# Kernel optimization log

Hardware: AMD Instinct MI355X
Metric: run time of the kernel (lower is better)

## Reference

```python
import jax, jax.numpy as jnp
import numpy as np

D = 512      # d_model
H = 8        # n_heads
DH = D // H  # d_head
WIN = 128    # window radius
FF = 4 * D   # ffn hidden
B, T = 4, 2048
EPS = 1e-5


def _ln(x, g, b):
    mu = jnp.mean(x, axis=-1, keepdims=True)
    var = jnp.mean((x - mu) ** 2, axis=-1, keepdims=True)
    return (x - mu) * jax.lax.rsqrt(var + EPS) * g + b


def _rope(x):
    # standard rotate-half RoPE over the full d_model dim (applied to ln(x)
    # before q/k/v projections, as in the source module)
    t, d = x.shape[-2], x.shape[-1]
    half = d // 2
    inv_freq = 1.0 / (10000.0 ** (jnp.arange(half, dtype=jnp.float32) / half))
    ang = jnp.arange(t, dtype=jnp.float32)[:, None] * inv_freq[None, :]  # (T, half)
    cos, sin = jnp.cos(ang), jnp.sin(ang)
    x1, x2 = x[..., :half], x[..., half:]
    return jnp.concatenate([x1 * cos - x2 * sin, x1 * sin + x2 * cos], axis=-1)


def setup_inputs() -> dict:
    key = jax.random.key(0)
    ks = jax.random.split(key, 16)
    s = 0.02
    inp = {
        "x": jax.random.normal(ks[0], (B, T, D), dtype=jnp.float32),
        "Wq": jax.random.normal(ks[1], (D, D), dtype=jnp.float32) * s,
        "bq": jnp.zeros((D,), jnp.float32),
        "Wk": jax.random.normal(ks[2], (D, D), dtype=jnp.float32) * s,
        "bk": jnp.zeros((D,), jnp.float32),
        "Wv": jax.random.normal(ks[3], (D, D), dtype=jnp.float32) * s,
        "bv": jnp.zeros((D,), jnp.float32),
        "Wo": jax.random.normal(ks[4], (D, D), dtype=jnp.float32) * s,
        "bo": jnp.zeros((D,), jnp.float32),
        "ln_g": jnp.ones((D,), jnp.float32),
        "ln_b": jnp.zeros((D,), jnp.float32),
        "ffln_g": jnp.ones((D,), jnp.float32),
        "ffln_b": jnp.zeros((D,), jnp.float32),
        "W1": jax.random.normal(ks[5], (D, FF), dtype=jnp.float32) * s,
        "b1": jnp.zeros((FF,), jnp.float32),
        "W2": jax.random.normal(ks[6], (FF, D), dtype=jnp.float32) * s,
        "b2": jnp.zeros((D,), jnp.float32),
    }
    return inp


def reference(x, Wq, bq, Wk, bk, Wv, bv, Wo, bo, ln_g, ln_b, ffln_g, ffln_b, W1, b1, W2, b2):
    b, t, d = x.shape
    h = _rope(_ln(x, ln_g, ln_b))
    q = (h @ Wq + bq).reshape(b, t, H, DH).transpose(0, 2, 1, 3)  # (B,H,T,DH)
    k = (h @ Wk + bk).reshape(b, t, H, DH).transpose(0, 2, 1, 3)
    v = (h @ Wv + bv).reshape(b, t, H, DH).transpose(0, 2, 1, 3)

    scores = jnp.einsum("bhqd,bhkd->bhqk", q, k) / jnp.sqrt(jnp.float32(DH))
    # Faithful to source local_mask semantics under torch SDPA bool-mask
    # convention (True = attend): attention is ALLOWED where |i-j| > window.
    idx = jnp.arange(t)
    allowed = jnp.abs(idx[:, None] - idx[None, :]) > WIN  # (T,T) bool
    scores = jnp.where(allowed, scores, -jnp.inf)
    attn = jax.nn.softmax(scores, axis=-1)
    o = jnp.einsum("bhqk,bhkd->bhqd", attn, v)
    o = o.transpose(0, 2, 1, 3).reshape(b, t, d)
    x = x + (o @ Wo + bo)

    # source applies self.ln AND the ff's internal LayerNorm back-to-back
    f = _ln(_ln(x, ln_g, ln_b), ffln_g, ffln_b)
    f = jax.nn.gelu(f @ W1 + b1, approximate=False) @ W2 + b2
    return x + f
```

## Files before the change

kernel.cpp:

```cpp
#include <hip/hip_runtime.h>
#include <cmath>

typedef __bf16 bf16x8 __attribute__((ext_vector_type(8)));
typedef float  f32x4  __attribute__((ext_vector_type(4)));
typedef float  f32x16 __attribute__((ext_vector_type(16)));
typedef int    i32x4  __attribute__((ext_vector_type(4)));

#define MFMA(a, b, c)   __builtin_amdgcn_mfma_f32_16x16x32_bf16((a), (b), (c), 0, 0, 0)
#define MFMA32(a, b, c) __builtin_amdgcn_mfma_f32_32x32x16_bf16((a), (b), (c), 0, 0, 0)

static __device__ __forceinline__ unsigned fbits(float f) {
  union { float f; unsigned u; } v; v.f = f; return v.u;
}
static __device__ __forceinline__ __bf16 f2bf(float f) {
  unsigned u = fbits(f);
  unsigned r = u + 0x7fffu + ((u >> 16) & 1u);
  union { unsigned short u; __bf16 b; } o; o.u = (unsigned short)(r >> 16);
  return o.b;
}
static __device__ __forceinline__ unsigned pack2rn(float a, float b) {
  unsigned ua = fbits(a); ua = ua + 0x7fffu + ((ua >> 16) & 1u);
  unsigned ub = fbits(b); ub = ub + 0x7fffu + ((ub >> 16) & 1u);
  return __builtin_amdgcn_perm(ub, ua, 0x07060302);
}

typedef const __attribute__((address_space(1))) void* gas_t;
typedef __attribute__((address_space(3))) void* las_t;
static __device__ __forceinline__ void load_lds16(const __bf16* g, __bf16* l) {
  __builtin_amdgcn_global_load_lds((gas_t)g, (las_t)l, 16, 0, 0);
}

__global__ __launch_bounds__(256) void k_pre(
    const float* __restrict__ Wq, const float* __restrict__ Wk,
    const float* __restrict__ Wv, const float* __restrict__ Wo,
    const float* __restrict__ W1, const float* __restrict__ W2,
    __bf16* __restrict__ wqkv, __bf16* __restrict__ wo,
    __bf16* __restrict__ w1t, __bf16* __restrict__ w2t,
    const float* __restrict__ x, const float* __restrict__ g,
    const float* __restrict__ b, __bf16* __restrict__ h) {
  if (blockIdx.x < 12288) {
    int idx = blockIdx.x * 256 + threadIdx.x;
    const float* src; __bf16* dst; int off, logK, N;
    if (idx < 1048576) {
      int which = idx >> 18; off = idx & 262143; logK = 9; N = 512;
      src = which == 0 ? Wq : which == 1 ? Wk : which == 2 ? Wv : Wo;
      dst = which < 3 ? wqkv + which * 262144 : wo;
    } else if (idx < 2097152) {
      off = idx - 1048576; logK = 9; N = 2048; src = W1; dst = w1t;
    } else {
      off = idx - 2097152; logK = 11; N = 512; src = W2; dst = w2t;
    }
    int n = off >> logK, k = off & ((1 << logK) - 1);
    dst[off] = f2bf(src[(size_t)k * N + n]);
    return;
  }
  int n = blockIdx.x - 12288, tid = threadIdx.x;
  const float* row = x + (size_t)n * 512;
  float v1 = row[tid], v2 = row[tid + 256];
  float s = v1 + v2, ss = v1 * v1 + v2 * v2;
  #pragma unroll
  for (int off = 1; off < 64; off <<= 1) { s += __shfl_xor(s, off, 64); ss += __shfl_xor(ss, off, 64); }
  __shared__ float red[2][4];
  if ((tid & 63) == 0) { red[0][tid >> 6] = s; red[1][tid >> 6] = ss; }
  __syncthreads();
  s  = red[0][0] + red[0][1] + red[0][2] + red[0][3];
  ss = red[1][0] + red[1][1] + red[1][2] + red[1][3];
  float mu = s * (1.f / 512.f);
  float var = ss * (1.f / 512.f) - mu * mu;
  float rs = rsqrtf(var + 1e-5f);
  float y1 = (v1 - mu) * rs * g[tid] + b[tid];
  float y2 = (v2 - mu) * rs * g[tid + 256] + b[tid + 256];
  int t = n & 2047;
  float inv = __expf(-(float)tid * 0.03597789207803197f);
  float ang = (float)t * inv;
  float sn, c;
  __sincosf(ang, &sn, &c);
  h[(size_t)n * 512 + tid]       = f2bf(y1 * c - y2 * sn);
  h[(size_t)n * 512 + tid + 256] = f2bf(y1 * sn + y2 * c);
}

template <int K>
static __device__ __forceinline__ void gemm128(const __bf16* __restrict__ A,
                                               const __bf16* __restrict__ Bt,
                                               f32x4 (&acc)[2][4]) {
  __shared__ __bf16 lA[128 * 64];
  __shared__ __bf16 lB[128 * 64];
  int bm = blockIdx.x & 63, bn = blockIdx.x >> 6;
  int tid = threadIdx.x, w = tid >> 6, lane = tid & 63;
  int l16 = lane & 15, quad = lane >> 4;
  int wr = (w & 3) * 32, wc = (w >> 2) * 64;
  int srow = w * 8 + (lane >> 3);
  int sg = (lane & 7) ^ (srow & 7);
  const __bf16* ga = A  + (size_t)(bm * 128 + srow) * K + sg * 8;
  const __bf16* gb = Bt + (size_t)(bn * 128 + srow) * K + sg * 8;
  __bf16* saw = lA + w * 512;
  __bf16* sbw = lB + w * 512;
  #pragma unroll
  for (int i = 0; i < 2; ++i)
    #pragma unroll
    for (int j = 0; j < 4; ++j) acc[i][j] = {0.f, 0.f, 0.f, 0.f};
  const size_t rstep = (size_t)64 * K;
  for (int k0 = 0; k0 < K; k0 += 64) {
    load_lds16(ga + k0,         saw);
    load_lds16(ga + k0 + rstep, saw + 4096);
    load_lds16(gb + k0,         sbw);
    load_lds16(gb + k0 + rstep, sbw + 4096);
    __syncthreads();
    #pragma unroll
    for (int kk = 0; kk < 2; ++kk) {
      int gg = kk * 4 + quad;
      bf16x8 af[2], bfr[4];
      #pragma unroll
      for (int i = 0; i < 2; ++i) {
        int row = wr + i * 16 + l16;
        __builtin_memcpy(&af[i], &lA[row * 64 + ((gg ^ (row & 7)) * 8)], 16);
      }
      #pragma unroll
      for (int j = 0; j < 4; ++j) {
        int row = wc + j * 16 + l16;
        __builtin_memcpy(&bfr[j], &lB[row * 64 + ((gg ^ (row & 7)) * 8)], 16);
      }
      #pragma unroll
      for (int i = 0; i < 2; ++i)
        #pragma unroll
        for (int j = 0; j < 4; ++j) acc[i][j] = MFMA(af[i], bfr[j], acc[i][j]);
    }
    __syncthreads();
  }
}

#define G128_EPILOG_IDX                                 \
  int bm = blockIdx.x & 63, bn = blockIdx.x >> 6;       \
  int lane = threadIdx.x & 63, w = threadIdx.x >> 6;    \
  int l16 = lane & 15, quad = lane >> 4;                \
  int wr = (w & 3) * 32, wc = (w >> 2) * 64;

__global__ __launch_bounds__(512) void k_gemm_qkv(const __bf16* __restrict__ A,
                                                  const __bf16* __restrict__ Bt,
                                                  const float* __restrict__ bq,
                                                  const float* __restrict__ bk,
                                                  const float* __restrict__ bv,
                                                  __bf16* __restrict__ qo,
                                                  __bf16* __restrict__ ko,
                                                  __bf16* __restrict__ vT) {
  f32x4 acc[2][4];
  gemm128<512>(A, Bt, acc);
  G128_EPILOG_IDX
  int proj = bn >> 2;
  const float* bias = proj == 0 ? bq : (proj == 1 ? bk : bv);
  float scale = proj == 0 ? 0.125f : 1.f;
  if (proj < 2) {
    __bf16* dst = proj == 0 ? qo : ko;
    #pragma unroll
    for (int i = 0; i < 2; ++i)
      #pragma unroll
      for (int j = 0; j < 4; ++j)
        #pragma unroll
        for (int r = 0; r < 4; ++r) {
          int c = (bn * 128 + wc + j * 16 + l16) & 511;
          int m = bm * 128 + wr + i * 16 + quad * 4 + r;
          int bI = m >> 11, t = m & 2047;
          int head = c >> 6, dh = c & 63;
          dst[(((size_t)bI * 8 + head) * 2048 + t) * 64 + dh] = f2bf((acc[i][j][r] + bias[c]) * scale);
        }
  } else {
    #pragma unroll
    for (int i = 0; i < 2; ++i)
      #pragma unroll
      for (int j = 0; j < 4; ++j)
        #pragma unroll
        for (int r = 0; r < 4; ++r) {
          int c = (bn * 128 + wc + j * 16 + l16) & 511;
          int m = bm * 128 + wr + i * 16 + quad * 4 + r;
          int bI = m >> 11, t = m & 2047;
          int head = c >> 6, dh = c & 63;
          vT[(((size_t)bI * 8 + head) * 64 + dh) * 2048 + t] = f2bf(acc[i][j][r] + bias[c]);
        }
  }
}

template <int K, typename EPI>
static __device__ __forceinline__ void gemm64sk(const __bf16* __restrict__ A,
                                                const __bf16* __restrict__ Bt,
                                                EPI epi) {
  __shared__ __align__(16) char smem[64 * 128 * 2 * 2];
  __bf16* lA = (__bf16*)smem;
  __bf16* lB = lA + 64 * 128;
  int bm = blockIdx.x & 127, bn = blockIdx.x >> 7;
  int tid = threadIdx.x, w = tid >> 6, lane = tid & 63;
  int l16 = lane & 15, quad = lane >> 4;
  int pos = w & 3, half = w >> 2;
  int wr = (pos >> 1) * 32, wc = (pos & 1) * 32;
  int srow = tid >> 4;
  int sg = (tid & 15) ^ (srow & 15);
  const __bf16* ga = A  + (size_t)(bm * 64 + srow) * K + sg * 8;
  const __bf16* gb = Bt + (size_t)(bn * 64 + srow) * K + sg * 8;
  __bf16* sa = lA + w * 512;
  __bf16* sb = lB + w * 512;
  f32x4 acc[2][2];
  #pragma unroll
  for (int i = 0; i < 2; ++i)
    #pragma unroll
    for (int j = 0; j < 2; ++j) acc[i][j] = {0.f, 0.f, 0.f, 0.f};
  const size_t rstep = (size_t)32 * K;
  for (int k0 = 0; k0 < K; k0 += 128) {
    load_lds16(ga + k0,         sa);
    load_lds16(ga + k0 + rstep, sa + 4096);
    load_lds16(gb + k0,         sb);
    load_lds16(gb + k0 + rstep, sb + 4096);
    __syncthreads();
    #pragma unroll
    for (int kk = 0; kk < 2; ++kk) {
      int gg = half * 8 + kk * 4 + quad;
      bf16x8 af[2], bfr[2];
      #pragma unroll
      for (int i = 0; i < 2; ++i) {
        int row = wr + i * 16 + l16;
        __builtin_memcpy(&af[i], &lA[row * 128 + ((gg ^ (row & 15)) * 8)], 16);
      }
      #pragma unroll
      for (int j = 0; j < 2; ++j) {
        int row = wc + j * 16 + l16;
        __builtin_memcpy(&bfr[j], &lB[row * 128 + ((gg ^ (row & 15)) * 8)], 16);
      }
      #pragma unroll
      for (int i = 0; i < 2; ++i)
        #pragma unroll
        for (int j = 0; j < 2; ++j) acc[i][j] = MFMA(af[i], bfr[j], acc[i][j]);
    }
    __syncthreads();
  }
  float (*cbuf)[64][17] = (float(*)[64][17])smem;
  if (half) {
    #pragma unroll
    for (int i = 0; i < 2; ++i)
      #pragma unroll
      for (int j = 0; j < 2; ++j)
        #pragma unroll
        for (int r = 0; r < 4; ++r) cbuf[pos][lane][(i * 2 + j) * 4 + r] = acc[i][j][r];
  }
  __syncthreads();
  if (!half) {
    #pragma unroll
    for (int i = 0; i < 2; ++i)
      #pragma unroll
      for (int j = 0; j < 2; ++j)
        #pragma unroll
        for (int r = 0; r < 4; ++r) {
          float v = acc[i][j][r] + cbuf[pos][lane][(i * 2 + j) * 4 + r];
          int m = bm * 64 + wr + i * 16 + quad * 4 + r;
          int n = bn * 64 + wc + j * 16 + l16;
          epi(m, n, v);
        }
  }
}

__global__ __launch_bounds__(512) void k_gemm_oproj(const __bf16* __restrict__ A,
                                                    const __bf16* __restrict__ Bt,
                                                    const float* __restrict__ bo,
                                                    const float* __restrict__ xin,
                                                    float* __restrict__ x2) {
  gemm64sk<512>(A, Bt, [&](int m, int n, float v) {
    size_t idx = (size_t)m * 512 + n;
    x2[idx] = xin[idx] + v + bo[n];
  });
}

__global__ __launch_bounds__(512) void k_gemm_ffn2(const __bf16* __restrict__ A,
                                                   const __bf16* __restrict__ Bt,
                                                   const float* __restrict__ b2,
                                                   const float* __restrict__ x2,
                                                   float* __restrict__ out) {
  gemm64sk<2048>(A, Bt, [&](int m, int n, float v) {
    size_t idx = (size_t)m * 512 + n;
    out[idx] = x2[idx] + v + b2[n];
  });
}

__global__ __launch_bounds__(512) void k_attn(const __bf16* __restrict__ q,
                                              const __bf16* __restrict__ k,
                                              const __bf16* __restrict__ vT,
                                              __bf16* __restrict__ o) {
  __shared__ __align__(16) __bf16 Kt[64 * 64];
  __shared__ __align__(16) __bf16 Vt[64 * 64];
  __shared__ float cbuf[4][64][17];
  int bh = blockIdx.x >> 4, qblk = blockIdx.x & 15;
  int tid = threadIdx.x, w = tid >> 6, lane = tid & 63;
  int l32 = lane & 31, h32 = lane >> 5;
  int qw = w & 3, half = w >> 2, hoff = half * 32;
  int qB = qblk * 128;
  int q0 = qB + qw * 32;
  int qglob = q0 + l32;
  const __bf16* qb = q + (size_t)bh * 2048 * 64;
  const __bf16* kb = k + (size_t)bh * 2048 * 64;
  const __bf16* vb = vT + (size_t)bh * 64 * 2048;
  bf16x8 aq[4];
  #pragma unroll
  for (int i = 0; i < 4; ++i)
    aq[i] = *(const bf16x8*)(qb + (size_t)qglob * 64 + i * 16 + h32 * 8);
  f32x16 on0 = {0,0,0,0,0,0,0,0,0,0,0,0,0,0,0,0};
  f32x16 on1 = {0,0,0,0,0,0,0,0,0,0,0,0,0,0,0,0};
  float lsum = 0.f;
  int srow = w * 8 + (lane >> 3);
  int sg = (lane & 7) ^ (srow & 7);
  const __bf16* gk = kb + (size_t)srow * 64 + sg * 8;
  const __bf16* gv = vb + (size_t)srow * 2048 + sg * 8;
  __bf16* skw = Kt + w * 512;
  __bf16* svw = Vt + w * 512;

  for (int it = 0; it < 32; ++it) {
    int kt64 = it * 64;
    if ((unsigned)(kt64 - qB) <= 64u) continue;
    load_lds16(gk + (size_t)kt64 * 64, skw);
    load_lds16(gv + kt64, svw);
    __syncthreads();
    int myk0 = kt64 + hoff;
    bool skip = (q0 + 31 - myk0 <= 128) && (myk0 + 31 - q0 <= 128);
    if (!skip) {
      bool need_mask = !((myk0 >= q0 + 160) || (myk0 <= q0 - 160));
      f32x16 sc = {0,0,0,0,0,0,0,0,0,0,0,0,0,0,0,0};
      int krow = hoff + l32;
      #pragma unroll
      for (int i = 0; i < 4; ++i) {
        int gg = i * 2 + h32;
        bf16x8 bk;
        __builtin_memcpy(&bk, &Kt[krow * 64 + ((gg ^ (krow & 7)) * 8)], 16);
        sc = MFMA32(bk, aq[i], sc);
      }
      unsigned pk[8];
      #pragma unroll
      for (int g2 = 0; g2 < 8; ++g2) {
        int r0 = 2 * g2;
        float p0 = __expf(sc[r0]);
        float p1 = __expf(sc[r0 + 1]);
        if (need_mask) {
          int k0l = (r0 & 3) + 8 * (r0 >> 2) + 4 * h32;
          if ((unsigned)(qglob - (myk0 + k0l) + 128) <= 256u) p0 = 0.f;
          if ((unsigned)(qglob - (myk0 + k0l + 1) + 128) <= 256u) p1 = 0.f;
        }
        lsum += p0 + p1;
        pk[g2] = __builtin_amdgcn_perm(fbits(p1), fbits(p0), 0x07060302);
      }
      unsigned ex[8];
      #pragma unroll
      for (int g2 = 0; g2 < 8; ++g2) ex[g2] = (unsigned)__shfl_xor((int)pk[g2], 32);
      #pragma unroll
      for (int kk = 0; kk < 2; ++kk) {
        int o4 = kk * 4;
        i32x4 fi;
        fi.x = (int)(h32 ? ex[o4 + 2] : pk[o4 + 0]);
        fi.y = (int)(h32 ? ex[o4 + 3] : pk[o4 + 1]);
        fi.z = (int)(h32 ? pk[o4 + 2] : ex[o4 + 0]);
        fi.w = (int)(h32 ? pk[o4 + 3] : ex[o4 + 1]);
        bf16x8 pf;
        __builtin_memcpy(&pf, &fi, 16);
        int gg = half * 4 + kk * 2 + h32;
        bf16x8 bv0, bv1;
        __builtin_memcpy(&bv0, &Vt[l32 * 64 + ((gg ^ (l32 & 7)) * 8)], 16);
        __builtin_memcpy(&bv1, &Vt[(32 + l32) * 64 + ((gg ^ (l32 & 7)) * 8)], 16);
        on0 = MFMA32(bv0, pf, on0);
        on1 = MFMA32(bv1, pf, on1);
      }
    }
    __syncthreads();
  }
  if (half) {
    for (int i = 0; i < 16; ++i) cbuf[qw][lane][i] = on0[i];
  }
  __syncthreads();
  if (!half) {
    for (int i = 0; i < 16; ++i) on0[i] += cbuf[qw][lane][i];
  }
  __syncthreads();
  if (half) {
    for (int i = 0; i < 16; ++i) cbuf[qw][lane][i] = on1[i];
  }
  __syncthreads();
  if (!half) {
    for (int i = 0; i < 16; ++i) on1[i] += cbuf[qw][lane][i];
  }
  __syncthreads();
  if (half) {
    cbuf[qw][lane][0] = lsum;
  }
  __syncthreads();
  if (!half) {
    float s = lsum + cbuf[qw][lane][0];
    s += __shfl_xor(s, 32);
    float rl = 1.f / s;
    int bI = bh >> 3, head = bh & 7;
    __bf16* obase = o + ((size_t)(bI * 2048 + qglob)) * 512 + head * 64 + 4 * h32;
    #pragma unroll
    for (int g2 = 0; g2 < 4; ++g2) {
      int r0 = 4 * g2;
      int2 v0, v1;
      v0.x = (int)pack2rn(on0[r0] * rl, on0[r0 + 1] * rl);
      v0.y = (int)pack2rn(on0[r0 + 2] * rl, on0[r0 + 3] * rl);
      v1.x = (int)pack2rn(on1[r0] * rl, on1[r0 + 1] * rl);
      v1.y = (int)pack2rn(on1[r0 + 2] * rl, on1[r0 + 3] * rl);
      *(int2*)(obase + 8 * g2) = v0;
      *(int2*)(obase + 32 + 8 * g2) = v1;
    }
  }
}

__global__ __launch_bounds__(256) void k_ln_ln(const float* __restrict__ x2,
                                               const float* __restrict__ g1v,
                                               const float* __restrict__ b1v,
                                               const float* __restrict__ g2v,
                                               const float* __restrict__ b2v,
                                               __bf16* __restrict__ fout) {
  int n = blockIdx.x, tid = threadIdx.x;
  const float* row = x2 + (size_t)n * 512;
  float v1 = row[tid], v2 = row[tid + 256];
  __shared__ float red[2][4];
  float s = v1 + v2, ss = v1 * v1 + v2 * v2;
  #pragma unroll
  for (int off = 1; off < 64; off <<= 1) { s += __shfl_xor(s, off, 64); ss += __shfl_xor(ss, off, 64); }
  if ((tid & 63) == 0) { red[0][tid >> 6] = s; red[1][tid >> 6] = ss; }
  __syncthreads();
  s  = red[0][0] + red[0][1] + red[0][2] + red[0][3];
  ss = red[1][0] + red[1][1] + red[1][2] + red[1][3];
  float mu = s * (1.f / 512.f), var = ss * (1.f / 512.f) - mu * mu;
  float rs = rsqrtf(var + 1e-5f);
  float y1 = (v1 - mu) * rs * g1v[tid] + b1v[tid];
  float y2 = (v2 - mu) * rs * g1v[tid + 256] + b1v[tid + 256];
  __syncthreads();
  s = y1 + y2; ss = y1 * y1 + y2 * y2;
  #pragma unroll
  for (int off = 1; off < 64; off <<= 1) { s += __shfl_xor(s, off, 64); ss += __shfl_xor(ss, off, 64); }
  if ((tid & 63) == 0) { red[0][tid >> 6] = s; red[1][tid >> 6] = ss; }
  __syncthreads();
  s  = red[0][0] + red[0][1] + red[0][2] + red[0][3];
  ss = red[1][0] + red[1][1] + red[1][2] + red[1][3];
  float mu2 = s * (1.f / 512.f), var2 = ss * (1.f / 512.f) - mu2 * mu2;
  float rs2 = rsqrtf(var2 + 1e-5f);
  fout[(size_t)n * 512 + tid]       = f2bf((y1 - mu2) * rs2 * g2v[tid] + b2v[tid]);
  fout[(size_t)n * 512 + tid + 256] = f2bf((y2 - mu2) * rs2 * g2v[tid + 256] + b2v[tid + 256]);
}

__global__ __launch_bounds__(512) void k_gemm_ffn1(const __bf16* __restrict__ A,
                                                   const __bf16* __restrict__ Bt,
                                                   const float* __restrict__ b1,
                                                   __bf16* __restrict__ g1) {
  f32x4 acc[2][4];
  gemm128<512>(A, Bt, acc);
  G128_EPILOG_IDX
  #pragma unroll
  for (int i = 0; i < 2; ++i)
    #pragma unroll
    for (int j = 0; j < 4; ++j)
      #pragma unroll
      for (int r = 0; r < 4; ++r) {
        int n = bn * 128 + wc + j * 16 + l16;
        int m = bm * 128 + wr + i * 16 + quad * 4 + r;
        float t = acc[i][j][r] + b1[n];
        float ge = 0.5f * t * (1.f + erff(t * 0.7071067811865475f));
        g1[(size_t)m * 2048 + n] = f2bf(ge);
      }
}

extern "C" void kernel_launch(void* const* d_in, const int* in_sizes, int n_in,
                              void* d_out, int out_size, void* d_ws, size_t ws_size,
                              hipStream_t stream) {
  (void)in_sizes; (void)n_in; (void)out_size; (void)ws_size;
  const float* x   = (const float*)d_in[0];
  const float* Wq  = (const float*)d_in[1];
  const float* bq  = (const float*)d_in[2];
  const float* Wk  = (const float*)d_in[3];
  const float* bk  = (const float*)d_in[4];
  const float* Wv  = (const float*)d_in[5];
  const float* bv  = (const float*)d_in[6];
  const float* Wo  = (const float*)d_in[7];
  const float* bo  = (const float*)d_in[8];
  const float* lng = (const float*)d_in[9];
  const float* lnb = (const float*)d_in[10];
  const float* ffg = (const float*)d_in[11];
  const float* ffb = (const float*)d_in[12];
  const float* W1  = (const float*)d_in[13];
  const float* b1  = (const float*)d_in[14];
  const float* W2  = (const float*)d_in[15];
  const float* b2  = (const float*)d_in[16];
  float* out = (float*)d_out;

  char* ws = (char*)d_ws;
  __bf16* h    = (__bf16*)(ws);
  __bf16* qb   = (__bf16*)(ws + (size_t)8 * 1024 * 1024);
  __bf16* kb   = (__bf16*)(ws + (size_t)16 * 1024 * 1024);
  __bf16* vT   = (__bf16*)(ws + (size_t)24 * 1024 * 1024);
  float*  x2   = (float*)(ws + (size_t)32 * 1024 * 1024);
  __bf16* fb   = (__bf16*)(ws + (size_t)48 * 1024 * 1024);
  __bf16* wqkv = (__bf16*)(ws + (size_t)56 * 1024 * 1024);
  __bf16* wo   = wqkv + 3 * 512 * 512;
  __bf16* w1t  = wo + 512 * 512;
  __bf16* w2t  = w1t + 512 * 2048;
  __bf16* g1   = (__bf16*)(ws);

  k_pre<<<12288 + 8192, 256, 0, stream>>>(Wq, Wk, Wv, Wo, W1, W2, wqkv, wo, w1t, w2t,
                                          x, lng, lnb, h);
  k_gemm_qkv<<<64 * 12, 512, 0, stream>>>(h, wqkv, bq, bk, bv, qb, kb, vT);
  k_attn<<<32 * 16, 512, 0, stream>>>(qb, kb, vT, h);
  k_gemm_oproj<<<128 * 8, 512, 0, stream>>>(h, wo, bo, x, x2);
  k_ln_ln<<<8192, 256, 0, stream>>>(x2, lng, lnb, ffg, ffb, fb);
  k_gemm_ffn1<<<64 * 16, 512, 0, stream>>>(fb, w1t, b1, g1);
  k_gemm_ffn2<<<128 * 8, 512, 0, stream>>>(g1, w2t, b2, x2, out);
}
```

Before: 277.0 us.

## Switch QKV and FFN1 GEMMs to 64-tile split-K kernel, bf16 residual, exp2 softmax

Drops the 128x128 GEMM path and runs the QKV and FFN1 projections through the 64x64 split-K GEMM with more blocks. The Q scale is folded into a log2(e)/8 factor so attention can use a native exp2 in place of __expf. The intermediate residual x2 is stored as bf16 rather than fp32, cutting traffic for the LN and FFN2 epilogues but adding rounding error to the residual stream. The smaller tiles raise block count and occupancy at the cost of less operand reuse per block.

```diff
diff --git a/kernel.cpp b/kernel.cpp
--- a/kernel.cpp
+++ b/kernel.cpp
@@ -22,6 +22,13 @@
   unsigned ua = fbits(a); ua = ua + 0x7fffu + ((ua >> 16) & 1u);
   unsigned ub = fbits(b); ub = ub + 0x7fffu + ((ub >> 16) & 1u);
   return __builtin_amdgcn_perm(ub, ua, 0x07060302);
+}
+static __device__ __forceinline__ float fexp2(float x) {
+#if __has_builtin(__builtin_amdgcn_exp2f)
+  return __builtin_amdgcn_exp2f(x);
+#else
+  return exp2f(x);
+#endif
 }
 
 typedef const __attribute__((address_space(1))) void* gas_t;
@@ -77,106 +84,6 @@
   __sincosf(ang, &sn, &c);
   h[(size_t)n * 512 + tid]       = f2bf(y1 * c - y2 * sn);
   h[(size_t)n * 512 + tid + 256] = f2bf(y1 * sn + y2 * c);
-}
-
-template <int K>
-static __device__ __forceinline__ void gemm128(const __bf16* __restrict__ A,
-                                               const __bf16* __restrict__ Bt,
-                                               f32x4 (&acc)[2][4]) {
-  __shared__ __bf16 lA[128 * 64];
-  __shared__ __bf16 lB[128 * 64];
-  int bm = blockIdx.x & 63, bn = blockIdx.x >> 6;
-  int tid = threadIdx.x, w = tid >> 6, lane = tid & 63;
-  int l16 = lane & 15, quad = lane >> 4;
-  int wr = (w & 3) * 32, wc = (w >> 2) * 64;
-  int srow = w * 8 + (lane >> 3);
-  int sg = (lane & 7) ^ (srow & 7);
-  const __bf16* ga = A  + (size_t)(bm * 128 + srow) * K + sg * 8;
-  const __bf16* gb = Bt + (size_t)(bn * 128 + srow) * K + sg * 8;
-  __bf16* saw = lA + w * 512;
-  __bf16* sbw = lB + w * 512;
-  #pragma unroll
-  for (int i = 0; i < 2; ++i)
-    #pragma unroll
-    for (int j = 0; j < 4; ++j) acc[i][j] = {0.f, 0.f, 0.f, 0.f};
-  const size_t rstep = (size_t)64 * K;
-  for (int k0 = 0; k0 < K; k0 += 64) {
-    load_lds16(ga + k0,         saw);
-    load_lds16(ga + k0 + rstep, saw + 4096);
-    load_lds16(gb + k0,         sbw);
-    load_lds16(gb + k0 + rstep, sbw + 4096);
-    __syncthreads();
-    #pragma unroll
-    for (int kk = 0; kk < 2; ++kk) {
-      int gg = kk * 4 + quad;
-      bf16x8 af[2], bfr[4];
-      #pragma unroll
-      for (int i = 0; i < 2; ++i) {
-        int row = wr + i * 16 + l16;
-        __builtin_memcpy(&af[i], &lA[row * 64 + ((gg ^ (row & 7)) * 8)], 16);
-      }
-      #pragma unroll
-      for (int j = 0; j < 4; ++j) {
-        int row = wc + j * 16 + l16;
-        __builtin_memcpy(&bfr[j], &lB[row * 64 + ((gg ^ (row & 7)) * 8)], 16);
-      }
-      #pragma unroll
-      for (int i = 0; i < 2; ++i)
-        #pragma unroll
-        for (int j = 0; j < 4; ++j) acc[i][j] = MFMA(af[i], bfr[j], acc[i][j]);
-    }
-    __syncthreads();
-  }
-}
-
-#define G128_EPILOG_IDX                                 \
-  int bm = blockIdx.x & 63, bn = blockIdx.x >> 6;       \
-  int lane = threadIdx.x & 63, w = threadIdx.x >> 6;    \
-  int l16 = lane & 15, quad = lane >> 4;                \
-  int wr = (w & 3) * 32, wc = (w >> 2) * 64;
-
-__global__ __launch_bounds__(512) void k_gemm_qkv(const __bf16* __restrict__ A,
-                                                  const __bf16* __restrict__ Bt,
-                                                  const float* __restrict__ bq,
-                                                  const float* __restrict__ bk,
-                                                  const float* __restrict__ bv,
-                                                  __bf16* __restrict__ qo,
-                                                  __bf16* __restrict__ ko,
-                                                  __bf16* __restrict__ vT) {
-  f32x4 acc[2][4];
-  gemm128<512>(A, Bt, acc);
-  G128_EPILOG_IDX
-  int proj = bn >> 2;
-  const float* bias = proj == 0 ? bq : (proj == 1 ? bk : bv);
-  float scale = proj == 0 ? 0.125f : 1.f;
-  if (proj < 2) {
-    __bf16* dst = proj == 0 ? qo : ko;
-    #pragma unroll
-    for (int i = 0; i < 2; ++i)
-      #pragma unroll
-      for (int j = 0; j < 4; ++j)
-        #pragma unroll
-        for (int r = 0; r < 4; ++r) {
-          int c = (bn * 128 + wc + j * 16 + l16) & 511;
-          int m = bm * 128 + wr + i * 16 + quad * 4 + r;
-          int bI = m >> 11, t = m & 2047;
-          int head = c >> 6, dh = c & 63;
-          dst[(((size_t)bI * 8 + head) * 2048 + t) * 64 + dh] = f2bf((acc[i][j][r] + bias[c]) * scale);
-        }
-  } else {
-    #pragma unroll
-    for (int i = 0; i < 2; ++i)
-      #pragma unroll
-      for (int j = 0; j < 4; ++j)
-        #pragma unroll
-        for (int r = 0; r < 4; ++r) {
-          int c = (bn * 128 + wc + j * 16 + l16) & 511;
-          int m = bm * 128 + wr + i * 16 + quad * 4 + r;
-          int bI = m >> 11, t = m & 2047;
-          int head = c >> 6, dh = c & 63;
-          vT[(((size_t)bI * 8 + head) * 64 + dh) * 2048 + t] = f2bf(acc[i][j][r] + bias[c]);
-        }
-  }
 }
 
 template <int K, typename EPI>
@@ -255,25 +162,58 @@
   }
 }
 
+__global__ __launch_bounds__(512) void k_gemm_qkv(const __bf16* __restrict__ A,
+                                                  const __bf16* __restrict__ Bt,
+                                                  const float* __restrict__ bq,
+                                                  const float* __restrict__ bk,
+                                                  const float* __restrict__ bv,
+                                                  __bf16* __restrict__ qo,
+                                                  __bf16* __restrict__ ko,
+                                                  __bf16* __restrict__ vT) {
+  gemm64sk<512>(A, Bt, [&](int m, int n, float v) {
+    int proj = n >> 9, c = n & 511;
+    int bI = m >> 11, t = m & 2047;
+    int head = c >> 6, dh = c & 63;
+    if (proj == 0) {
+      qo[(((size_t)bI * 8 + head) * 2048 + t) * 64 + dh] = f2bf((v + bq[c]) * 0.18033688011112042f);
+    } else if (proj == 1) {
+      ko[(((size_t)bI * 8 + head) * 2048 + t) * 64 + dh] = f2bf(v + bk[c]);
+    } else {
+      vT[(((size_t)bI * 8 + head) * 64 + dh) * 2048 + t] = f2bf(v + bv[c]);
+    }
+  });
+}
+
 __global__ __launch_bounds__(512) void k_gemm_oproj(const __bf16* __restrict__ A,
                                                     const __bf16* __restrict__ Bt,
                                                     const float* __restrict__ bo,
                                                     const float* __restrict__ xin,
-                                                    float* __restrict__ x2) {
+                                                    __bf16* __restrict__ x2) {
   gemm64sk<512>(A, Bt, [&](int m, int n, float v) {
     size_t idx = (size_t)m * 512 + n;
-    x2[idx] = xin[idx] + v + bo[n];
+    x2[idx] = f2bf(xin[idx] + v + bo[n]);
+  });
+}
+
+__global__ __launch_bounds__(512) void k_gemm_ffn1(const __bf16* __restrict__ A,
+                                                   const __bf16* __restrict__ Bt,
+                                                   const float* __restrict__ b1,
+                                                   __bf16* __restrict__ g1) {
+  gemm64sk<512>(A, Bt, [&](int m, int n, float v) {
+    float t = v + b1[n];
+    float ge = 0.5f * t * (1.f + erff(t * 0.7071067811865475f));
+    g1[(size_t)m * 2048 + n] = f2bf(ge);
   });
 }
 
 __global__ __launch_bounds__(512) void k_gemm_ffn2(const __bf16* __restrict__ A,
                                                    const __bf16* __restrict__ Bt,
                                                    const float* __restrict__ b2,
-                                                   const float* __restrict__ x2,
+                                                   const __bf16* __restrict__ x2,
                                                    float* __restrict__ out) {
   gemm64sk<2048>(A, Bt, [&](int m, int n, float v) {
     size_t idx = (size_t)m * 512 + n;
-    out[idx] = x2[idx] + v + b2[n];
+    out[idx] = (float)x2[idx] + v + b2[n];
   });
 }
 
@@ -331,8 +271,8 @@
       #pragma unroll
       for (int g2 = 0; g2 < 8; ++g2) {
         int r0 = 2 * g2;
-        float p0 = __expf(sc[r0]);
-        float p1 = __expf(sc[r0 + 1]);
+        float p0 = fexp2(sc[r0]);
+        float p1 = fexp2(sc[r0 + 1]);
         if (need_mask) {
           int k0l = (r0 & 3) + 8 * (r0 >> 2) + 4 * h32;
           if ((unsigned)(qglob - (myk0 + k0l) + 128) <= 256u) p0 = 0.f;
@@ -404,14 +344,14 @@
   }
 }
 
-__global__ __launch_bounds__(256) void k_ln_ln(const float* __restrict__ x2,
+__global__ __launch_bounds__(256) void k_ln_ln(const __bf16* __restrict__ x2,
                                                const float* __restrict__ g1v,
                                                const float* __restrict__ b1v,
                                                const float* __restrict__ g2v,
                                                const float* __restrict__ b2v,
                                                __bf16* __restrict__ fout) {
   int n = blockIdx.x, tid = threadIdx.x;
-  const float* row = x2 + (size_t)n * 512;
+  const __bf16* row = x2 + (size_t)n * 512;
   float v1 = row[tid], v2 = row[tid + 256];
   __shared__ float red[2][4];
   float s = v1 + v2, ss = v1 * v1 + v2 * v2;
@@ -437,27 +377,6 @@
   float rs2 = rsqrtf(var2 + 1e-5f);
   fout[(size_t)n * 512 + tid]       = f2bf((y1 - mu2) * rs2 * g2v[tid] + b2v[tid]);
   fout[(size_t)n * 512 + tid + 256] = f2bf((y2 - mu2) * rs2 * g2v[tid + 256] + b2v[tid + 256]);
-}
-
-__global__ __launch_bounds__(512) void k_gemm_ffn1(const __bf16* __restrict__ A,
-                                                   const __bf16* __restrict__ Bt,
-                                                   const float* __restrict__ b1,
-                                                   __bf16* __restrict__ g1) {
-  f32x4 acc[2][4];
-  gemm128<512>(A, Bt, acc);
-  G128_EPILOG_IDX
-  #pragma unroll
-  for (int i = 0; i < 2; ++i)
-    #pragma unroll
-    for (int j = 0; j < 4; ++j)
-      #pragma unroll
-      for (int r = 0; r < 4; ++r) {
-        int n = bn * 128 + wc + j * 16 + l16;
-        int m = bm * 128 + wr + i * 16 + quad * 4 + r;
-        float t = acc[i][j][r] + b1[n];
-        float ge = 0.5f * t * (1.f + erff(t * 0.7071067811865475f));
-        g1[(size_t)m * 2048 + n] = f2bf(ge);
-      }
 }
 
 extern "C" void kernel_launch(void* const* d_in, const int* in_sizes, int n_in,
@@ -488,7 +407,7 @@
   __bf16* qb   = (__bf16*)(ws + (size_t)8 * 1024 * 1024);
   __bf16* kb   = (__bf16*)(ws + (size_t)16 * 1024 * 1024);
   __bf16* vT   = (__bf16*)(ws + (size_t)24 * 1024 * 1024);
-  float*  x2   = (float*)(ws + (size_t)32 * 1024 * 1024);
+  __bf16* x2   = (__bf16*)(ws + (size_t)32 * 1024 * 1024);
   __bf16* fb   = (__bf16*)(ws + (size_t)48 * 1024 * 1024);
   __bf16* wqkv = (__bf16*)(ws + (size_t)56 * 1024 * 1024);
   __bf16* wo   = wqkv + 3 * 512 * 512;
@@ -498,10 +417,10 @@
 
   k_pre<<<12288 + 8192, 256, 0, stream>>>(Wq, Wk, Wv, Wo, W1, W2, wqkv, wo, w1t, w2t,
                                           x, lng, lnb, h);
-  k_gemm_qkv<<<64 * 12, 512, 0, stream>>>(h, wqkv, bq, bk, bv, qb, kb, vT);
+  k_gemm_qkv<<<24 * 128, 512, 0, stream>>>(h, wqkv, bq, bk, bv, qb, kb, vT);
   k_attn<<<32 * 16, 512, 0, stream>>>(qb, kb, vT, h);
-  k_gemm_oproj<<<128 * 8, 512, 0, stream>>>(h, wo, bo, x, x2);
+  k_gemm_oproj<<<8 * 128, 512, 0, stream>>>(h, wo, bo, x, x2);
   k_ln_ln<<<8192, 256, 0, stream>>>(x2, lng, lnb, ffg, ffb, fb);
-  k_gemm_ffn1<<<64 * 16, 512, 0, stream>>>(fb, w1t, b1, g1);
-  k_gemm_ffn2<<<128 * 8, 512, 0, stream>>>(g1, w2t, b2, x2, out);
-}
+  k_gemm_ffn1<<<32 * 128, 512, 0, stream>>>(fb, w1t, b1, g1);
+  k_gemm_ffn2<<<8 * 128, 512, 0, stream>>>(g1, w2t, b2, x2, out);
+}
```

Result: no change. 281.3 us (+1.6%).
